# Optimization experiments

Measured on AMD Instinct MI355X. Metric: run time of the kernel, lower is better.

Reference implementation:

```python
import jax, jax.numpy as jnp
import numpy as np

N_NODES = 100000
N_EDGES = 1600000
IN_F, HID, OUT_F = 64, 64, 64
NUM_RELS, NUM_BASES = 4, 2


def _glorot(key, shape):
    fan_in, fan_out = shape[-2], shape[-1]
    lim = jnp.sqrt(6.0 / (fan_in + fan_out))
    return jax.random.uniform(key, shape, jnp.float32, -lim, lim)


def setup_inputs() -> dict:
    key = jax.random.key(0)
    ks = jax.random.split(key, 16)
    inp = {
        "features": jax.random.normal(ks[0], (N_NODES, IN_F), jnp.float32),
        "src": jax.random.randint(ks[1], (N_EDGES,), 0, N_NODES, jnp.int32),
        "dst": jax.random.randint(ks[2], (N_EDGES,), 0, N_NODES, jnp.int32),
        "edge_types": jax.random.randint(ks[3], (N_EDGES,), 0, NUM_RELS, jnp.int32),
    }
    dims = [(IN_F, HID), (HID, HID), (HID, OUT_F)]
    for i, (di, do) in enumerate(dims, start=1):
        inp[f"bases{i}"] = _glorot(ks[3 + 3 * i], (NUM_BASES, di, do))
        inp[f"comp{i}"] = _glorot(ks[4 + 3 * i], (NUM_RELS, NUM_BASES))
        inp[f"loop_w{i}"] = _glorot(ks[5 + 3 * i], (di, do))
        inp[f"bias{i}"] = jnp.zeros((do,), jnp.float32)
    inp["pred_w"] = _glorot(ks[13], (OUT_F, 1))
    inp["pred_b"] = jnp.zeros((1,), jnp.float32)
    return inp


def rel_graph_conv(x, src, dst, etypes, bases, comp, loop_w, bias):
    # basis-composed per-node transform: [N, B, out]
    xb = jnp.einsum('ni,bio->nbo', x, bases)
    # per-edge message: combine basis outputs of source node with comp[etype]
    msg = jnp.einsum('eb,ebo->eo', comp[etypes], xb[src])  # [E, out]
    agg = jax.ops.segment_sum(msg, dst, num_segments=x.shape[0])
    return agg + x @ loop_w + bias


def reference(features, src, dst, edge_types,
              bases1, comp1, loop_w1, bias1,
              bases2, comp2, loop_w2, bias2,
              bases3, comp3, loop_w3, bias3,
              pred_w, pred_b):
    x = jax.nn.relu(rel_graph_conv(features, src, dst, edge_types, bases1, comp1, loop_w1, bias1))
    # dropout is identity in eval mode
    x = jax.nn.relu(rel_graph_conv(x, src, dst, edge_types, bases2, comp2, loop_w2, bias2))
    x = jax.nn.relu(rel_graph_conv(x, src, dst, edge_types, bases3, comp3, loop_w3, bias3))
    logits = (x @ pred_w + pred_b)[:, 0]
    return jax.nn.sigmoid(logits)
```

## Files before the change

kernel.cpp:

```cpp
#include <hip/hip_runtime.h>
#include <hip/hip_bf16.h>
#include <hip/hip_fp16.h>


#define NB1 196
#define NBLK1 256
#define BUCKET_SHIFT 9
#define WT_LD 200

typedef unsigned short ushort_t;
typedef _Float16 h8 __attribute__((ext_vector_type(8)));
typedef float f32x4 __attribute__((ext_vector_type(4)));

__device__ inline ushort_t f2h(float f) {
  __half h = __float2half_rn(f);
  return *(ushort_t*)&h;
}
__device__ inline float h2f(ushort_t u) {
  __half h = *(__half*)&u;
  return __half2float(h);
}

__device__ inline int block_incl_scan_256(int v, int* wsums) {
  int lane = threadIdx.x & 63, wid = threadIdx.x >> 6;
  int s = v;
#pragma unroll
  for (int off = 1; off < 64; off <<= 1) {
    int u = __shfl_up(s, off, 64);
    if (lane >= off) s += u;
  }
  if (lane == 63) wsums[wid] = s;
  __syncthreads();
  if (threadIdx.x == 0) {
    int a = 0;
#pragma unroll
    for (int w = 0; w < 4; ++w) { int t = wsums[w]; wsums[w] = a; a += t; }
  }
  __syncthreads();
  return s + wsums[wid];
}

__global__ void __launch_bounds__(256) k_l1hist(const int* __restrict__ dst,
                                                int* __restrict__ H, int E, int chunk) {
  __shared__ int h[NB1];
  int t = threadIdx.x;
  if (t < NB1) h[t] = 0;
  __syncthreads();
  int beg = blockIdx.x * chunk;
  int end = min(beg + chunk, E);
  for (int i = beg + t; i < end; i += 256) atomicAdd(&h[dst[i] >> BUCKET_SHIFT], 1);
  __syncthreads();
  if (t < NB1) H[blockIdx.x * NB1 + t] = h[t];
}

__global__ void __launch_bounds__(256) k_colscan(int* __restrict__ H,
                                                 int* __restrict__ total) {
  __shared__ int wsums[4];
  int b = blockIdx.x;
  int t = threadIdx.x;
  int v = H[t * NB1 + b];
  int s = block_incl_scan_256(v, wsums);
  H[t * NB1 + b] = s - v;
  if (t == 255) total[b] = s;
}

__global__ void __launch_bounds__(256) k_basescan(const int* __restrict__ total,
                                                  int* __restrict__ bucket_base,
                                                  int* __restrict__ row_off, int N) {
  __shared__ int wsums[4];
  int t = threadIdx.x;
  int v = (t < NB1) ? total[t] : 0;
  int s = block_incl_scan_256(v, wsums);
  if (t < NB1) bucket_base[t] = s - v;
  if (t == 255) { bucket_base[NB1] = s; row_off[N] = s; }
}

__global__ void __launch_bounds__(256) k_scatter1(
    const int* __restrict__ src, const int* __restrict__ dst,
    const int* __restrict__ et, const int* __restrict__ H,
    const int* __restrict__ bucket_base, int* __restrict__ epk1,
    int E, int chunk) {
  __shared__ int cur[NB1];
  int t = threadIdx.x;
  if (t < NB1) cur[t] = bucket_base[t] + H[blockIdx.x * NB1 + t];
  __syncthreads();
  int beg = blockIdx.x * chunk;
  int end = min(beg + chunk, E);
  for (int i = beg + t; i < end; i += 256) {
    int d = dst[i];
    int b = d >> BUCKET_SHIFT;
    int p = atomicAdd(&cur[b], 1);
    epk1[p] = src[i] | (et[i] << 17) | ((d & 511) << 19);
  }
}

__global__ void __launch_bounds__(256) k_bucket(
    const int* __restrict__ epk1, const int* __restrict__ bucket_base,
    int* __restrict__ epk, int* __restrict__ row_off, int N) {
  __shared__ int hist[512];
  __shared__ int cur[512];
  __shared__ int wsums[4];
  int b = blockIdx.x;
  int t = threadIdx.x;
  int ebase = bucket_base[b], eend = bucket_base[b + 1];
  hist[t] = 0; hist[t + 256] = 0;
  __syncthreads();
  for (int i = ebase + t; i < eend; i += 256) atomicAdd(&hist[epk1[i] >> 19], 1);
  __syncthreads();
  int h0 = hist[2 * t], h1 = hist[2 * t + 1];
  int pair = h0 + h1;
  int incl = block_incl_scan_256(pair, wsums);
  int e0 = incl - pair;
  cur[2 * t] = ebase + e0;
  cur[2 * t + 1] = ebase + e0 + h0;
  int n0 = (b << BUCKET_SHIFT) + 2 * t;
  if (n0 < N) row_off[n0] = ebase + e0;
  if (n0 + 1 < N) row_off[n0 + 1] = ebase + e0 + h0;
  __syncthreads();
  for (int i = ebase + t; i < eend; i += 256) {
    int pk = epk1[i];
    int p = atomicAdd(&cur[pk >> 19], 1);
    epk[p] = pk;
  }
}

__global__ void __launch_bounds__(256) k_quant(const float* __restrict__ in,
                                               ushort_t* __restrict__ out, int n4) {
  int i = blockIdx.x * blockDim.x + threadIdx.x;
  if (i < n4) {
    float4 v = ((const float4*)in)[i];
    ushort4 q;
    q.x = f2h(v.x); q.y = f2h(v.y);
    q.z = f2h(v.z); q.w = f2h(v.w);
    ((ushort4*)out)[i] = q;
  }
}

__global__ void __launch_bounds__(256) k_aggregate(
    const ushort_t* __restrict__ xq, const int* __restrict__ row_off,
    const int* __restrict__ epk, const float* __restrict__ comp,
    ushort_t* __restrict__ Zh, int N) {
  __shared__ float s_comp[8];
  if (threadIdx.x < 8) s_comp[threadIdx.x] = comp[threadIdx.x];
  __syncthreads();
  int node = blockIdx.x * 4 + (threadIdx.x >> 6);
  int lane = threadIdx.x & 63;
  if (node >= N) return;
  int beg = row_off[node], end = row_off[node + 1];
  float z0 = 0.f, z1 = 0.f;
  int e = beg;
  for (; e + 7 < end; e += 8) {
    int pk[8];
    float xv[8];
#pragma unroll
    for (int u = 0; u < 8; ++u) pk[u] = epk[e + u];
#pragma unroll
    for (int u = 0; u < 8; ++u)
      xv[u] = h2f(xq[(size_t)(pk[u] & 0x1FFFF) * 64 + lane]);
#pragma unroll
    for (int u = 0; u < 8; ++u) {
      int r = (pk[u] >> 17) & 3;
      z0 = fmaf(s_comp[r * 2 + 0], xv[u], z0);
      z1 = fmaf(s_comp[r * 2 + 1], xv[u], z1);
    }
  }
  for (; e < end; ++e) {
    int pk = epk[e];
    int s = pk & 0x1FFFF, r = (pk >> 17) & 3;
    float xv = h2f(xq[(size_t)s * 64 + lane]);
    z0 = fmaf(s_comp[r * 2 + 0], xv, z0);
    z1 = fmaf(s_comp[r * 2 + 1], xv, z1);
  }
  Zh[(size_t)node * 128 + lane] = f2h(z0);
  Zh[(size_t)node * 128 + 64 + lane] = f2h(z1);
}

__global__ void __launch_bounds__(256) k_gemm_mfma(
    const ushort_t* __restrict__ Zh, const ushort_t* __restrict__ xq,
    const float* __restrict__ bases, const float* __restrict__ loopw,
    const float* __restrict__ bias, ushort_t* __restrict__ xqOut,
    const float* __restrict__ pw, const float* __restrict__ pb,
    float* __restrict__ predOut, int N) {
  __shared__ ushort_t sWh[64 * WT_LD];
  __shared__ ushort_t sWr[64 * WT_LD];
  int t = threadIdx.x;
  int w = t >> 6, l = t & 63;
  int lr = l & 15, lg = l >> 4;
  int row0 = blockIdx.x * 64 + w * 16;

  int arow = row0 + lr;
  bool rok = arow < N;
  h8 a[6];
#pragma unroll
  for (int kb = 0; kb < 6; ++kb) {
    int k0 = kb * 32 + lg * 8;
    uint4 u = make_uint4(0, 0, 0, 0);
    if (rok) {
      if (kb < 4) u = *(const uint4*)(Zh + (size_t)arow * 128 + k0);
      else        u = *(const uint4*)(xq + (size_t)arow * 64 + (k0 - 128));
    }
    a[kb] = *(h8*)&u;
  }

#pragma unroll 4
  for (int i = 0; i < 48; ++i) {
    int idx = i * 256 + t;
    int k = idx >> 6, c = idx & 63;
    float wv = (k < 128) ? bases[idx] : loopw[idx - 8192];
    ushort_t hh = f2h(wv);
    sWh[c * WT_LD + k] = hh;
    sWr[c * WT_LD + k] = f2h(wv - h2f(hh));
  }
  __syncthreads();

  f32x4 acc[4];
#pragma unroll
  for (int c = 0; c < 4; ++c) acc[c] = (f32x4){0.f, 0.f, 0.f, 0.f};
#pragma unroll
  for (int c = 0; c < 4; ++c) {
    int col = c * 16 + lr;
    const ushort_t* bh = sWh + col * WT_LD + lg * 8;
    const ushort_t* br = sWr + col * WT_LD + lg * 8;
#pragma unroll
    for (int kb = 0; kb < 6; ++kb) {
      h8 vb = *(const h8*)(bh + kb * 32);
      acc[c] = __builtin_amdgcn_mfma_f32_16x16x32_f16(a[kb], vb, acc[c], 0, 0, 0);
      h8 vr = *(const h8*)(br + kb * 32);
      acc[c] = __builtin_amdgcn_mfma_f32_16x16x32_f16(a[kb], vr, acc[c], 0, 0, 0);
    }
  }

  float o_[4][4];
#pragma unroll
  for (int c = 0; c < 4; ++c) {
    float bv = bias[c * 16 + lr];
#pragma unroll
    for (int r = 0; r < 4; ++r) o_[c][r] = fmaxf(acc[c][r] + bv, 0.f);
  }
  if (xqOut) {
#pragma unroll
    for (int c = 0; c < 4; ++c) {
      int col = c * 16 + lr;
#pragma unroll
      for (int r = 0; r < 4; ++r) {
        int grow = row0 + lg * 4 + r;
        if (grow < N)
          xqOut[(size_t)grow * 64 + col] = f2h(o_[c][r]);
      }
    }
  }
  if (predOut) {
    float pwv[4];
#pragma unroll
    for (int c = 0; c < 4; ++c) pwv[c] = pw[c * 16 + lr];
#pragma unroll
    for (int r = 0; r < 4; ++r) {
      float s_ = o_[0][r] * pwv[0] + o_[1][r] * pwv[1] +
                 o_[2][r] * pwv[2] + o_[3][r] * pwv[3];
#pragma unroll
      for (int off = 1; off < 16; off <<= 1) s_ += __shfl_xor(s_, off, 64);
      int grow = row0 + lg * 4 + r;
      if (lr == 0 && grow < N) {
        float logit = s_ + pb[0];
        predOut[grow] = 1.f / (1.f + expf(-logit));
      }
    }
  }
}

extern "C" void kernel_launch(void* const* d_in, const int* in_sizes, int n_in,
                              void* d_out, int out_size, void* d_ws, size_t ws_size,
                              hipStream_t stream) {
  const float* features = (const float*)d_in[0];
  const int* src = (const int*)d_in[1];
  const int* dst = (const int*)d_in[2];
  const int* et  = (const int*)d_in[3];
  const float* bases[3] = {(const float*)d_in[4], (const float*)d_in[8],  (const float*)d_in[12]};
  const float* comp[3]  = {(const float*)d_in[5], (const float*)d_in[9],  (const float*)d_in[13]};
  const float* loopw[3] = {(const float*)d_in[6], (const float*)d_in[10], (const float*)d_in[14]};
  const float* biasp[3] = {(const float*)d_in[7], (const float*)d_in[11], (const float*)d_in[15]};
  const float* pred_w = (const float*)d_in[16];
  const float* pred_b = (const float*)d_in[17];

  const int N = in_sizes[0] / 64;
  const int E = in_sizes[1];

  char* ws = (char*)d_ws;
  size_t off = 0;
  auto take = [&](size_t bytes) {
    char* p = ws + off;
    off += (bytes + 255) & ~(size_t)255;
    return p;
  };
  int*      row_off     = (int*)     take((size_t)(N + 1) * 4);
  int*      H           = (int*)     take((size_t)NBLK1 * NB1 * 4);
  int*      total       = (int*)     take((size_t)NB1 * 4);
  int*      bucket_base = (int*)     take((size_t)(NB1 + 1) * 4);
  int*      epk         = (int*)     take((size_t)(E + 8) * 4);
  ushort_t* Zh          = (ushort_t*)take((size_t)N * 128 * 2);
  ushort_t* xqA         = (ushort_t*)take((size_t)N * 64 * 2);
  ushort_t* xqB         = (ushort_t*)take((size_t)N * 64 * 2);
  int*      epk1        = (int*)Zh;
  (void)ws_size;

  int chunk = (E + NBLK1 - 1) / NBLK1;
  k_l1hist  <<<NBLK1, 256, 0, stream>>>(dst, H, E, chunk);
  k_colscan <<<NB1,   256, 0, stream>>>(H, total);
  k_basescan<<<1,     256, 0, stream>>>(total, bucket_base, row_off, N);
  k_scatter1<<<NBLK1, 256, 0, stream>>>(src, dst, et, H, bucket_base, epk1, E, chunk);
  k_bucket  <<<NB1,   256, 0, stream>>>(epk1, bucket_base, epk, row_off, N);

  k_quant<<<(N * 16 + 255) / 256, 256, 0, stream>>>(features, xqA, N * 16);

  ushort_t* bufs[2] = {xqA, xqB};
  int agg_grid = (N + 3) / 4;
  int gemm_grid = (N + 63) / 64;
  for (int l = 0; l < 3; ++l) {
    k_aggregate<<<agg_grid, 256, 0, stream>>>(bufs[l & 1], row_off, epk,
                                              comp[l], Zh, N);
    bool last = (l == 2);
    k_gemm_mfma<<<gemm_grid, 256, 0, stream>>>(
        Zh, bufs[l & 1], bases[l], loopw[l], biasp[l],
        last ? nullptr : bufs[(l + 1) & 1],
        pred_w, pred_b, last ? (float*)d_out : nullptr, N);
  }
}
```

Measured before the change: 331.5 us.

## Pad CSR rows to multiples of eight and software-pipeline edge gathers across nodes

The bucketing pass now pads each node's edge list to a multiple of 8 using dummy entries whose relation index points to zero coefficients, and records a separate row_end array. The aggregation kernel gives each wavefront 8 consecutive nodes and double-buffers 8-edge gather batches across node boundaries, so the next batch's loads are in flight while the current one is accumulated. This removes the scalar tail loop and is meant to hide gather latency, at the cost of extra wasted gathers on padding (every node gets at least 8 slots), a larger edge buffer, and fewer wavefronts in flight.

New measurement: 276.6 us (median of 2 runs). 1.2x faster.

```diff
diff --git a/kernel.cpp b/kernel.cpp
--- a/kernel.cpp
+++ b/kernel.cpp
@@ -6,7 +6,10 @@
 #define NB1 196
 #define NBLK1 256
 #define BUCKET_SHIFT 9
+#define PAD_ALLOW 4096
 #define WT_LD 200
+#define DUMMY_PK (4 << 17)
+#define WNODES 8
 
 typedef unsigned short ushort_t;
 typedef _Float16 h8 __attribute__((ext_vector_type(8)));
@@ -65,14 +68,13 @@
 }
 
 __global__ void __launch_bounds__(256) k_basescan(const int* __restrict__ total,
-                                                  int* __restrict__ bucket_base,
-                                                  int* __restrict__ row_off, int N) {
+                                                  int* __restrict__ bucket_base) {
   __shared__ int wsums[4];
   int t = threadIdx.x;
   int v = (t < NB1) ? total[t] : 0;
   int s = block_incl_scan_256(v, wsums);
   if (t < NB1) bucket_base[t] = s - v;
-  if (t == 255) { bucket_base[NB1] = s; row_off[N] = s; }
+  if (t == 255) bucket_base[NB1] = s;
 }
 
 __global__ void __launch_bounds__(256) k_scatter1(
@@ -90,36 +92,43 @@
     int d = dst[i];
     int b = d >> BUCKET_SHIFT;
     int p = atomicAdd(&cur[b], 1);
-    epk1[p] = src[i] | (et[i] << 17) | ((d & 511) << 19);
+    epk1[p] = src[i] | (et[i] << 17) | ((d & 511) << 20);
   }
 }
 
 __global__ void __launch_bounds__(256) k_bucket(
     const int* __restrict__ epk1, const int* __restrict__ bucket_base,
-    int* __restrict__ epk, int* __restrict__ row_off, int N) {
+    int* __restrict__ epk, int* __restrict__ row_off,
+    int* __restrict__ row_end, int N) {
   __shared__ int hist[512];
   __shared__ int cur[512];
   __shared__ int wsums[4];
   int b = blockIdx.x;
   int t = threadIdx.x;
   int ebase = bucket_base[b], eend = bucket_base[b + 1];
+  int pb = ebase + b * PAD_ALLOW;
   hist[t] = 0; hist[t + 256] = 0;
   __syncthreads();
-  for (int i = ebase + t; i < eend; i += 256) atomicAdd(&hist[epk1[i] >> 19], 1);
+  for (int i = ebase + t; i < eend; i += 256) atomicAdd(&hist[epk1[i] >> 20], 1);
   __syncthreads();
   int h0 = hist[2 * t], h1 = hist[2 * t + 1];
-  int pair = h0 + h1;
+  int pd0 = (h0 == 0) ? 8 : ((h0 + 7) & ~7);
+  int pd1 = (h1 == 0) ? 8 : ((h1 + 7) & ~7);
+  int pair = pd0 + pd1;
   int incl = block_incl_scan_256(pair, wsums);
-  int e0 = incl - pair;
-  cur[2 * t] = ebase + e0;
-  cur[2 * t + 1] = ebase + e0 + h0;
+  int pe0 = incl - pair;
+  int s0 = pb + pe0, s1 = pb + pe0 + pd0;
+  cur[2 * t] = s0;
+  cur[2 * t + 1] = s1;
   int n0 = (b << BUCKET_SHIFT) + 2 * t;
-  if (n0 < N) row_off[n0] = ebase + e0;
-  if (n0 + 1 < N) row_off[n0 + 1] = ebase + e0 + h0;
+  if (n0 < N)     { row_off[n0] = s0;     row_end[n0] = s0 + pd0; }
+  if (n0 + 1 < N) { row_off[n0 + 1] = s1; row_end[n0 + 1] = s1 + pd1; }
+  for (int p = s0 + h0; p < s0 + pd0; ++p) epk[p] = DUMMY_PK;
+  for (int p = s1 + h1; p < s1 + pd1; ++p) epk[p] = DUMMY_PK;
   __syncthreads();
   for (int i = ebase + t; i < eend; i += 256) {
     int pk = epk1[i];
-    int p = atomicAdd(&cur[pk >> 19], 1);
+    int p = atomicAdd(&cur[pk >> 20], 1);
     epk[p] = pk;
   }
 }
@@ -138,41 +147,70 @@
 
 __global__ void __launch_bounds__(256) k_aggregate(
     const ushort_t* __restrict__ xq, const int* __restrict__ row_off,
-    const int* __restrict__ epk, const float* __restrict__ comp,
-    ushort_t* __restrict__ Zh, int N) {
-  __shared__ float s_comp[8];
-  if (threadIdx.x < 8) s_comp[threadIdx.x] = comp[threadIdx.x];
-  __syncthreads();
-  int node = blockIdx.x * 4 + (threadIdx.x >> 6);
+    const int* __restrict__ row_end, const int* __restrict__ epk,
+    const float* __restrict__ comp, ushort_t* __restrict__ Zh, int N) {
+  __shared__ float s_comp[10];
+  if (threadIdx.x < 10)
+    s_comp[threadIdx.x] = (threadIdx.x < 8) ? comp[threadIdx.x] : 0.f;
+  __syncthreads();
   int lane = threadIdx.x & 63;
-  if (node >= N) return;
-  int beg = row_off[node], end = row_off[node + 1];
+  int wnode0 = (blockIdx.x * 4 + (threadIdx.x >> 6)) * WNODES;
+  if (wnode0 >= N) return;
+  int wnode1 = min(wnode0 + WNODES, N);
+
+  int nj = wnode0;
+  int ej = row_off[nj], ejEnd = row_end[nj];
+
+  int pkA[8], pkB[8];
+  ushort_t xvA[8], xvB[8];
+  int nodeA = wnode0, nodeB = wnode0;
+
+#define ISSUE(PK, XV, NODE)                                                 \
+  {                                                                         \
+    NODE = nj;                                                              \
+    _Pragma("unroll") for (int u = 0; u < 8; ++u) PK[u] = epk[ej + u];      \
+    _Pragma("unroll") for (int u = 0; u < 8; ++u)                           \
+        XV[u] = xq[(size_t)(PK[u] & 0x1FFFF) * 64 + lane];                  \
+    ej += 8;                                                                \
+    if (ej >= ejEnd) {                                                      \
+      if (nj + 1 < wnode1) { ++nj; ej = row_off[nj]; ejEnd = row_end[nj]; } \
+      else nj = -1;                                                         \
+    }                                                                       \
+  }
+
+  int ncons = wnode0;
   float z0 = 0.f, z1 = 0.f;
-  int e = beg;
-  for (; e + 7 < end; e += 8) {
-    int pk[8];
-    float xv[8];
-#pragma unroll
-    for (int u = 0; u < 8; ++u) pk[u] = epk[e + u];
-#pragma unroll
-    for (int u = 0; u < 8; ++u)
-      xv[u] = h2f(xq[(size_t)(pk[u] & 0x1FFFF) * 64 + lane]);
-#pragma unroll
-    for (int u = 0; u < 8; ++u) {
-      int r = (pk[u] >> 17) & 3;
-      z0 = fmaf(s_comp[r * 2 + 0], xv[u], z0);
-      z1 = fmaf(s_comp[r * 2 + 1], xv[u], z1);
-    }
-  }
-  for (; e < end; ++e) {
-    int pk = epk[e];
-    int s = pk & 0x1FFFF, r = (pk >> 17) & 3;
-    float xv = h2f(xq[(size_t)s * 64 + lane]);
-    z0 = fmaf(s_comp[r * 2 + 0], xv, z0);
-    z1 = fmaf(s_comp[r * 2 + 1], xv, z1);
-  }
-  Zh[(size_t)node * 128 + lane] = f2h(z0);
-  Zh[(size_t)node * 128 + 64 + lane] = f2h(z1);
+
+#define CONSUME(PK, XV, NODE)                                               \
+  {                                                                         \
+    if (NODE != ncons) {                                                    \
+      Zh[(size_t)ncons * 128 + lane] = f2h(z0);                             \
+      Zh[(size_t)ncons * 128 + 64 + lane] = f2h(z1);                        \
+      z0 = 0.f; z1 = 0.f; ncons = NODE;                                     \
+    }                                                                       \
+    _Pragma("unroll") for (int u = 0; u < 8; ++u) {                         \
+      int r = (PK[u] >> 17) & 7;                                            \
+      float xf = h2f(XV[u]);                                                \
+      z0 = fmaf(s_comp[r * 2 + 0], xf, z0);                                 \
+      z1 = fmaf(s_comp[r * 2 + 1], xf, z1);                                 \
+    }                                                                       \
+  }
+
+  ISSUE(pkA, xvA, nodeA);
+  for (;;) {
+    bool haveB = (nj >= 0);
+    if (haveB) ISSUE(pkB, xvB, nodeB);
+    CONSUME(pkA, xvA, nodeA);
+    if (!haveB) break;
+    bool haveA = (nj >= 0);
+    if (haveA) ISSUE(pkA, xvA, nodeA);
+    CONSUME(pkB, xvB, nodeB);
+    if (!haveA) break;
+  }
+  Zh[(size_t)ncons * 128 + lane] = f2h(z0);
+  Zh[(size_t)ncons * 128 + 64 + lane] = f2h(z1);
+#undef ISSUE
+#undef CONSUME
 }
 
 __global__ void __launch_bounds__(256) k_gemm_mfma(
@@ -293,10 +331,11 @@
     return p;
   };
   int*      row_off     = (int*)     take((size_t)(N + 1) * 4);
+  int*      row_end     = (int*)     take((size_t)N * 4);
   int*      H           = (int*)     take((size_t)NBLK1 * NB1 * 4);
   int*      total       = (int*)     take((size_t)NB1 * 4);
   int*      bucket_base = (int*)     take((size_t)(NB1 + 1) * 4);
-  int*      epk         = (int*)     take((size_t)(E + 8) * 4);
+  int*      epk         = (int*)     take((size_t)(E + NB1 * PAD_ALLOW + 8) * 4);
   ushort_t* Zh          = (ushort_t*)take((size_t)N * 128 * 2);
   ushort_t* xqA         = (ushort_t*)take((size_t)N * 64 * 2);
   ushort_t* xqB         = (ushort_t*)take((size_t)N * 64 * 2);
@@ -306,18 +345,18 @@
   int chunk = (E + NBLK1 - 1) / NBLK1;
   k_l1hist  <<<NBLK1, 256, 0, stream>>>(dst, H, E, chunk);
   k_colscan <<<NB1,   256, 0, stream>>>(H, total);
-  k_basescan<<<1,     256, 0, stream>>>(total, bucket_base, row_off, N);
+  k_basescan<<<1,     256, 0, stream>>>(total, bucket_base);
   k_scatter1<<<NBLK1, 256, 0, stream>>>(src, dst, et, H, bucket_base, epk1, E, chunk);
-  k_bucket  <<<NB1,   256, 0, stream>>>(epk1, bucket_base, epk, row_off, N);
+  k_bucket  <<<NB1,   256, 0, stream>>>(epk1, bucket_base, epk, row_off, row_end, N);
 
   k_quant<<<(N * 16 + 255) / 256, 256, 0, stream>>>(features, xqA, N * 16);
 
   ushort_t* bufs[2] = {xqA, xqB};
-  int agg_grid = (N + 3) / 4;
+  int agg_grid = (N + 4 * WNODES - 1) / (4 * WNODES);
   int gemm_grid = (N + 63) / 64;
   for (int l = 0; l < 3; ++l) {
-    k_aggregate<<<agg_grid, 256, 0, stream>>>(bufs[l & 1], row_off, epk,
-                                              comp[l], Zh, N);
+    k_aggregate<<<agg_grid, 256, 0, stream>>>(bufs[l & 1], row_off, row_end,
+                                              epk, comp[l], Zh, N);
     bool last = (l == 2);
     k_gemm_mfma<<<gemm_grid, 256, 0, stream>>>(
         Zh, bufs[l & 1], bases[l], loopw[l], biasp[l],
```
